# Kernel tuning notes

Hardware: AMD Instinct MI355X
Metric: run time of the kernel (lower is better)

## Reference

```python
import jax, jax.numpy as jnp
import numpy as np

N_HIDDEN = 8
N_CLASSES = 10
TIME_STEPS = 28
INPUT_DIM = 28
FORGET_BIAS = 1.0


def setup_inputs() -> dict:
    key = jax.random.key(0)
    k1, k2, k3, k4 = jax.random.split(key, 4)
    B = 32768
    x = jax.random.normal(k1, (B, TIME_STEPS, INPUT_DIM), dtype=jnp.float32)
    # BasicLSTMCell kernel: [input_dim + hidden, 4*hidden], gate order i, j, f, o
    W_lstm = jax.random.normal(k2, (INPUT_DIM + N_HIDDEN, 4 * N_HIDDEN), dtype=jnp.float32) * 0.1
    b_lstm = jnp.zeros((4 * N_HIDDEN,), dtype=jnp.float32)  # TF zero-init bias
    out_weights = jax.random.normal(k3, (N_HIDDEN, N_CLASSES), dtype=jnp.float32)
    out_biases = jax.random.normal(k4, (N_CLASSES,), dtype=jnp.float32)
    return {"x": x, "W_lstm": W_lstm, "b_lstm": b_lstm,
            "out_weights": out_weights, "out_biases": out_biases}


def reference(x, W_lstm, b_lstm, out_weights, out_biases):
    B = x.shape[0]

    def step(carry, xt):
        c, h = carry
        gates = jnp.concatenate([xt, h], axis=-1) @ W_lstm + b_lstm  # [B, 4H]
        i, j, f, o = jnp.split(gates, 4, axis=-1)  # BasicLSTMCell order: i, j, f, o
        new_c = c * jax.nn.sigmoid(f + FORGET_BIAS) + jax.nn.sigmoid(i) * jnp.tanh(j)
        new_h = jnp.tanh(new_c) * jax.nn.sigmoid(o)
        return (new_c, new_h), None

    xs = jnp.swapaxes(x, 0, 1)  # [T, B, input_dim]
    init = (jnp.zeros((B, N_HIDDEN), x.dtype), jnp.zeros((B, N_HIDDEN), x.dtype))
    (_, last_h), _ = jax.lax.scan(step, init, xs)
    logits = last_h @ out_weights + out_biases  # [B, n_classes]
    return logits
```

## Files before the change

kernel.cpp:

```cpp
#include <hip/hip_runtime.h>


#define TSTEPS 28
#define DIN    28
#define NH     8
#define NG     32
#define NC     10
#define NROWS  36

__device__ __forceinline__ float fast_exp2(float x) {
    return __builtin_amdgcn_exp2f(x);
}
__device__ __forceinline__ float fast_rcp(float x) {
    return __builtin_amdgcn_rcpf(x);
}
__device__ __forceinline__ float fast_sigmoid(float z) {
    return fast_rcp(1.0f + fast_exp2(-1.4426950408889634f * z));
}
__device__ __forceinline__ float fast_tanh(float z) {
    return 1.0f - 2.0f * fast_rcp(1.0f + fast_exp2(2.8853900817779268f * z));
}

__global__ __launch_bounds__(256, 2) void lstm_kernel(
    const float* __restrict__ x,
    const float* __restrict__ W,
    const float* __restrict__ bias,
    const float* __restrict__ Wout,
    const float* __restrict__ bout,
    float* __restrict__ out)
{
    const int tid  = blockIdx.x * 256 + threadIdx.x;
    const int e    = tid >> 3;
    const int u    = tid & 7;
    const int lane = threadIdx.x & 63;
    const int base8 = lane & ~7;

    const float* xb = x + (size_t)e * (TSTEPS * DIN);

    float Wr[NROWS][4];
#pragma unroll
    for (int k = 0; k < NROWS; ++k) {
#pragma unroll
        for (int gt = 0; gt < 4; ++gt)
            Wr[k][gt] = W[k * NG + gt * NH + u];
    }
    float bg[4];
#pragma unroll
    for (int gt = 0; gt < 4; ++gt) bg[gt] = bias[gt * NH + u];

    float c = 0.0f;
    float hall[NH];
#pragma unroll
    for (int j = 0; j < NH; ++j) hall[j] = 0.0f;

    float4 xq[7];
    {
        const float4* xv = (const float4*)xb;
#pragma unroll
        for (int i = 0; i < 7; ++i) xq[i] = xv[i];
    }

#pragma unroll 1
    for (int t = 0; t < TSTEPS; ++t) {
        float xt[DIN];
#pragma unroll
        for (int i = 0; i < 7; ++i) {
            xt[4*i+0] = xq[i].x; xt[4*i+1] = xq[i].y;
            xt[4*i+2] = xq[i].z; xt[4*i+3] = xq[i].w;
        }
        if (t + 1 < TSTEPS) {
            const float4* xv = (const float4*)(xb + (t + 1) * DIN);
#pragma unroll
            for (int i = 0; i < 7; ++i) xq[i] = xv[i];
        }

        float g[4];
#pragma unroll
        for (int gt = 0; gt < 4; ++gt) g[gt] = bg[gt];

#pragma unroll
        for (int k = 0; k < DIN; ++k) {
#pragma unroll
            for (int gt = 0; gt < 4; ++gt)
                g[gt] = fmaf(xt[k], Wr[k][gt], g[gt]);
        }
#pragma unroll
        for (int k = 0; k < NH; ++k) {
#pragma unroll
            for (int gt = 0; gt < 4; ++gt)
                g[gt] = fmaf(hall[k], Wr[DIN + k][gt], g[gt]);
        }

        float ig = fast_sigmoid(g[0]);
        float jg = fast_tanh(g[1]);
        float fg = fast_sigmoid(g[2] + 1.0f);
        float og = fast_sigmoid(g[3]);
        c = c * fg + ig * jg;
        float hu = fast_tanh(c) * og;

#pragma unroll
        for (int j = 0; j < NH; ++j)
            hall[j] = __shfl(hu, base8 + j, 64);
    }

    float acc = bout[u];
#pragma unroll
    for (int k = 0; k < NH; ++k)
        acc = fmaf(hall[k], Wout[k * NC + u], acc);
    out[(size_t)e * NC + u] = acc;

    if (u < 2) {
        float acc1 = bout[NH + u];
#pragma unroll
        for (int k = 0; k < NH; ++k)
            acc1 = fmaf(hall[k], Wout[k * NC + NH + u], acc1);
        out[(size_t)e * NC + NH + u] = acc1;
    }
}

extern "C" void kernel_launch(void* const* d_in, const int* in_sizes, int n_in,
                              void* d_out, int out_size, void* d_ws, size_t ws_size,
                              hipStream_t stream) {
    const float* x    = (const float*)d_in[0];
    const float* W    = (const float*)d_in[1];
    const float* b    = (const float*)d_in[2];
    const float* Wout = (const float*)d_in[3];
    const float* bout = (const float*)d_in[4];
    float* out = (float*)d_out;

    const int B = in_sizes[0] / (TSTEPS * DIN);
    const int threads = B * NH;
    const int block = 256;
    const int grid = threads / block;
    lstm_kernel<<<grid, block, 0, stream>>>(x, W, b, Wout, bout, out);
}
```

Baseline: 177.7 us.

## Split LSTM gates across 16 threads per sample to cut registers and raise occupancy

Each batch element is now handled by 16 threads instead of 8, and each thread computes two gate columns instead of four, so it holds 72 weight registers instead of 144. Gate pairs are exchanged with an xor shuffle so both half-groups can compute the cell update redundantly. Launch bounds rise to 4 blocks per CU, and the software prefetch of the next timestep's input is dropped in favour of a direct load each step. The cost is twice the threads, duplicated x loads and nonlinearity work across the two half-groups, an extra shuffle per step, and no explicit prefetch.

```diff
diff --git a/kernel.cpp b/kernel.cpp
--- a/kernel.cpp
+++ b/kernel.cpp
@@ -21,7 +21,7 @@
     return 1.0f - 2.0f * fast_rcp(1.0f + fast_exp2(2.8853900817779268f * z));
 }
 
-__global__ __launch_bounds__(256, 2) void lstm_kernel(
+__global__ __launch_bounds__(256, 4) void lstm_kernel(
     const float* __restrict__ x,
     const float* __restrict__ W,
     const float* __restrict__ bias,
@@ -29,92 +29,79 @@
     const float* __restrict__ bout,
     float* __restrict__ out)
 {
-    const int tid  = blockIdx.x * 256 + threadIdx.x;
-    const int e    = tid >> 3;
-    const int u    = tid & 7;
-    const int lane = threadIdx.x & 63;
-    const int base8 = lane & ~7;
+    const int tid    = blockIdx.x * 256 + threadIdx.x;
+    const int e      = tid >> 4;
+    const int p      = tid & 15;
+    const int lane   = threadIdx.x & 63;
+    const int base16 = lane & 48;
+    const bool low   = (p < NH);
 
     const float* xb = x + (size_t)e * (TSTEPS * DIN);
 
-    float Wr[NROWS][4];
+    float Wr0[NROWS], Wr1[NROWS];
 #pragma unroll
     for (int k = 0; k < NROWS; ++k) {
+        Wr0[k] = W[k * NG + p];
+        Wr1[k] = W[k * NG + 16 + p];
+    }
 #pragma unroll
-        for (int gt = 0; gt < 4; ++gt)
-            Wr[k][gt] = W[k * NG + gt * NH + u];
+    for (int k = 0; k < NROWS; ++k) {
+        asm volatile("" : "+v"(Wr0[k]), "+v"(Wr1[k]));
     }
-    float bg[4];
-#pragma unroll
-    for (int gt = 0; gt < 4; ++gt) bg[gt] = bias[gt * NH + u];
+
+    float bg0 = bias[p];
+    float bg1 = bias[16 + p];
 
     float c = 0.0f;
     float hall[NH];
 #pragma unroll
     for (int j = 0; j < NH; ++j) hall[j] = 0.0f;
 
-    float4 xq[7];
-    {
-        const float4* xv = (const float4*)xb;
-#pragma unroll
-        for (int i = 0; i < 7; ++i) xq[i] = xv[i];
-    }
-
 #pragma unroll 1
     for (int t = 0; t < TSTEPS; ++t) {
-        float xt[DIN];
-#pragma unroll
-        for (int i = 0; i < 7; ++i) {
-            xt[4*i+0] = xq[i].x; xt[4*i+1] = xq[i].y;
-            xt[4*i+2] = xq[i].z; xt[4*i+3] = xq[i].w;
-        }
-        if (t + 1 < TSTEPS) {
-            const float4* xv = (const float4*)(xb + (t + 1) * DIN);
+        float4 xq[7];
+        {
+            const float4* xv = (const float4*)(xb + t * DIN);
 #pragma unroll
             for (int i = 0; i < 7; ++i) xq[i] = xv[i];
         }
 
-        float g[4];
-#pragma unroll
-        for (int gt = 0; gt < 4; ++gt) g[gt] = bg[gt];
+        float g0 = bg0, g1 = bg1;
 
 #pragma unroll
-        for (int k = 0; k < DIN; ++k) {
-#pragma unroll
-            for (int gt = 0; gt < 4; ++gt)
-                g[gt] = fmaf(xt[k], Wr[k][gt], g[gt]);
+        for (int i = 0; i < 7; ++i) {
+            g0 = fmaf(xq[i].x, Wr0[4*i+0], g0);  g1 = fmaf(xq[i].x, Wr1[4*i+0], g1);
+            g0 = fmaf(xq[i].y, Wr0[4*i+1], g0);  g1 = fmaf(xq[i].y, Wr1[4*i+1], g1);
+            g0 = fmaf(xq[i].z, Wr0[4*i+2], g0);  g1 = fmaf(xq[i].z, Wr1[4*i+2], g1);
+            g0 = fmaf(xq[i].w, Wr0[4*i+3], g0);  g1 = fmaf(xq[i].w, Wr1[4*i+3], g1);
         }
 #pragma unroll
         for (int k = 0; k < NH; ++k) {
-#pragma unroll
-            for (int gt = 0; gt < 4; ++gt)
-                g[gt] = fmaf(hall[k], Wr[DIN + k][gt], g[gt]);
+            g0 = fmaf(hall[k], Wr0[DIN + k], g0);
+            g1 = fmaf(hall[k], Wr1[DIN + k], g1);
         }
 
-        float ig = fast_sigmoid(g[0]);
-        float jg = fast_tanh(g[1]);
-        float fg = fast_sigmoid(g[2] + 1.0f);
-        float og = fast_sigmoid(g[3]);
-        c = c * fg + ig * jg;
-        float hu = fast_tanh(c) * og;
+        float pg0 = __shfl_xor(g0, 8);
+        float pg1 = __shfl_xor(g1, 8);
+        float ig = low ? g0 : pg0;
+        float fg = low ? g1 : pg1;
+        float jg = low ? pg0 : g0;
+        float og = low ? pg1 : g1;
+
+        c = c * fast_sigmoid(fg + 1.0f) + fast_sigmoid(ig) * fast_tanh(jg);
+        float hu = fast_tanh(c) * fast_sigmoid(og);
 
 #pragma unroll
         for (int j = 0; j < NH; ++j)
-            hall[j] = __shfl(hu, base8 + j, 64);
+            hall[j] = __shfl(hu, base16 + j, 64);
     }
 
-    float acc = bout[u];
-#pragma unroll
-    for (int k = 0; k < NH; ++k)
-        acc = fmaf(hall[k], Wout[k * NC + u], acc);
-    out[(size_t)e * NC + u] = acc;
-
-    if (u < 2) {
-        float acc1 = bout[NH + u];
+    if (p < NC) {
+        float acc = bout[p];
 #pragma unroll
         for (int k = 0; k < NH; ++k)
-            acc1 = fmaf(hall[k], Wout[k * NC + NH + u], acc1);
-        out[(size_t)e * NC + NH + u] = acc1;
+            acc = fmaf(hall[k], Wout[k * NC + p], acc);
+        out[(size_t)e * NC + p] = acc;
     }
 }
 
@@ -129,7 +116,7 @@
     float* out = (float*)d_out;
 
     const int B = in_sizes[0] / (TSTEPS * DIN);
-    const int threads = B * NH;
+    const int threads = B * 16;
     const int block = 256;
     const int grid = threads / block;
     lstm_kernel<<<grid, block, 0, stream>>>(x, W, b, Wout, bout, out);
```

After: 215.6 us. 21.3% more time.
